# Optimization experiments

Hardware: AMD Instinct MI355X
Metric: run time of the kernel (lower is better)

Reference implementation:

```python
import jax, jax.numpy as jnp
import numpy as np

WINDOW = 32          # window_size
NUM_EIG = 8          # num_eigenvalues
EPS_NORM = 1e-8
EPS_DIV = 1e-8


def setup_inputs() -> dict:
    key = jax.random.key(0)
    h = jax.random.normal(key, (32, 4096, 1024), dtype=jnp.float32)
    return {"h": h}


def reference(h):
    batch, seq_len, hidden_dim = h.shape
    start = max(0, seq_len // 2 - 16)
    # [B, W, D] local window (fully in-bounds since seq_len >= window)
    w = jax.lax.dynamic_slice_in_dim(h, start, WINDOW, axis=1)
    wc = w - w.mean(axis=1, keepdims=True)                      # center over window
    wn = wc / (jnp.linalg.norm(wc, axis=2, keepdims=True) + EPS_NORM)
    # [B, W, W] local covariance (row-normalized gram)
    C = jnp.einsum('bwd,bvd->bwv', wn, wn)
    # batched symmetric eigendecomposition, ascending -> descending
    eigs = jnp.linalg.eigvalsh(C)[:, ::-1]                      # [B, W]
    e = eigs[:, :NUM_EIG + 1]                                    # top 9
    spectral_gap = e[:, NUM_EIG - 1] - e[:, NUM_EIG]             # lam_8 - lam_9
    decay_rate = (e[:, 0] - e[:, NUM_EIG]) / (NUM_EIG + 1)
    trace = jnp.trace(C, axis1=1, axis2=2)
    lambda_min = e[:, NUM_EIG] + 1e-8
    topo_term = jnp.maximum(spectral_gap / (decay_rate + EPS_DIV), 0.0)
    geo_term = lambda_min / (trace + EPS_DIV)
    gcve_scores = topo_term + geo_term                           # [B]
    fracture_scores = jnp.zeros_like(gcve_scores)                # phi_fn is None
    total_pressure = gcve_scores + fracture_scores
    return gcve_scores, fracture_scores, total_pressure
```

## Files before the change

kernel.cpp:

```cpp
#include <hip/hip_runtime.h>
#include <math.h>


namespace {
constexpr int HID = 1024;
constexpr int SEQ = 4096;
constexpr int START = 2032;
constexpr int NSWEEP = 8;

__device__ __forceinline__ void pairpq(int r, int m, int& p, int& q) {
    if (m == 0) { p = 31; q = r % 31; }
    else        { p = (r + m) % 31; q = (r + 31 - m) % 31; }
}
}

__global__ __launch_bounds__(256, 1)
void gyroid_probe_kernel(const float* __restrict__ h, float* __restrict__ out) {
    const int b = blockIdx.x;
    const int t = threadIdx.x;
    const float4* __restrict__ base4 =
        (const float4*)(h + ((size_t)b * SEQ + (size_t)START) * (size_t)HID);

    __shared__ float C[32][33];
    __shared__ __align__(16) float wcbuf[32][264];
    __shared__ float nsq[32];
    __shared__ float inv[32];
    __shared__ float csb[32];
    __shared__ float diag[32];
    __shared__ float misc[4];

    for (int i = t; i < 32 * 33; i += 256) (&C[0][0])[i] = 0.0f;
    if (t < 32) nsq[t] = 0.0f;
    if (t < 4)  misc[t] = 0.0f;
    __syncthreads();

    float4 sum4 = make_float4(0.f, 0.f, 0.f, 0.f);
    #pragma unroll
    for (int w = 0; w < 32; ++w) {
        float4 x = base4[w * 256 + t];
        sum4.x += x.x; sum4.y += x.y; sum4.z += x.z; sum4.w += x.w;
    }
    const float4 mean4 = make_float4(sum4.x * 0.03125f, sum4.y * 0.03125f,
                                     sum4.z * 0.03125f, sum4.w * 0.03125f);

    #pragma unroll
    for (int wi = 0; wi < 32; ++wi) {
        const int w = (wi + (t & 31)) & 31;
        float4 x = base4[w * 256 + t];
        const float dx = x.x - mean4.x, dy = x.y - mean4.y;
        const float dz = x.z - mean4.z, dw = x.w - mean4.w;
        atomicAdd(&nsq[w], dx * dx + dy * dy + dz * dz + dw * dw);
    }
    __syncthreads();

    const int tile = t & 15, kw = t >> 4;
    const int ti = tile >> 2, tj = tile & 3;
    float acc[8][8];
    #pragma unroll
    for (int i = 0; i < 8; ++i)
        #pragma unroll
        for (int j = 0; j < 8; ++j) acc[i][j] = 0.f;

    for (int g = 0; g < 4; ++g) {
        if ((t >> 6) == g) {
            const int col = t & 63;
            #pragma unroll
            for (int w = 0; w < 32; ++w) {
                float4 x = base4[w * 256 + t];
                float4 wc = make_float4(x.x - mean4.x, x.y - mean4.y,
                                        x.z - mean4.z, x.w - mean4.w);
                *(float4*)&wcbuf[w][col * 4] = wc;
            }
        }
        __syncthreads();
        #pragma unroll
        for (int k4 = 0; k4 < 4; ++k4) {
            const int k = kw * 16 + k4 * 4;
            float4 av[8], bv[8];
            #pragma unroll
            for (int i = 0; i < 8; ++i) av[i] = *(const float4*)&wcbuf[ti + 4 * i][k];
            #pragma unroll
            for (int j = 0; j < 8; ++j) bv[j] = *(const float4*)&wcbuf[tj + 4 * j][k];
            #pragma unroll
            for (int i = 0; i < 8; ++i)
                #pragma unroll
                for (int j = 0; j < 8; ++j)
                    acc[i][j] += av[i].x * bv[j].x + av[i].y * bv[j].y
                               + av[i].z * bv[j].z + av[i].w * bv[j].w;
        }
        __syncthreads();
    }

    #pragma unroll
    for (int i = 0; i < 8; ++i)
        #pragma unroll
        for (int j = 0; j < 8; ++j)
            atomicAdd(&C[ti + 4 * i][tj + 4 * j], acc[i][j]);
    __syncthreads();

    if (t < 32) inv[t] = 1.0f / (sqrtf(nsq[t]) + 1e-8f);
    __syncthreads();
    for (int i = t; i < 1024; i += 256) {
        const int w = i >> 5, v = i & 31;
        C[w][v] *= inv[w] * inv[v];
    }
    __syncthreads();
    if (t < 32) atomicAdd(&misc[0], C[t][t]);
    __syncthreads();

    for (int sweep = 0; sweep < NSWEEP; ++sweep) {
        for (int r = 0; r < 31; ++r) {
            if (t < 16) {
                int p, q; pairpq(r, t, p, q);
                const float app = C[p][p], aqq = C[q][q], apq = C[p][q];
                float cc = 1.f, ss = 0.f;
                if (fabsf(apq) > 1e-12f) {
                    const float tau = (aqq - app) / (2.f * apq);
                    float tt = 1.f / (fabsf(tau) + sqrtf(1.f + tau * tau));
                    if (tau < 0.f) tt = -tt;
                    cc = rsqrtf(1.f + tt * tt);
                    ss = tt * cc;
                }
                csb[t] = cc; csb[16 + t] = ss;
            }
            __syncthreads();
            {
                const int u = t >> 4, v = t & 15;
                int pu, qu, pv, qv;
                pairpq(r, u, pu, qu);
                pairpq(r, v, pv, qv);
                const float cu = csb[u], su = csb[16 + u];
                const float cv = csb[v], sv = csb[16 + v];
                const float a = C[pu][pv], bb = C[pu][qv];
                const float d = C[qu][pv], e = C[qu][qv];
                const float a1 = a * cv - bb * sv, b1 = a * sv + bb * cv;
                const float d1 = d * cv - e * sv,  e1 = d * sv + e * cv;
                C[pu][pv] = cu * a1 - su * d1;
                C[qu][pv] = su * a1 + cu * d1;
                C[pu][qv] = cu * b1 - su * e1;
                C[qu][qv] = su * b1 + cu * e1;
            }
            __syncthreads();
        }
    }

    if (t < 32) diag[t] = C[t][t];
    __syncthreads();
    if (t < 32) {
        const float dj = diag[t];
        int rank = 0;
        #pragma unroll
        for (int i = 0; i < 32; ++i) {
            const float di = diag[i];
            rank += (di > dj || (di == dj && i < t)) ? 1 : 0;
        }
        if (rank == 0) misc[1] = dj;
        if (rank == 7) misc[2] = dj;
        if (rank == 8) misc[3] = dj;
    }
    __syncthreads();

    if (t == 0) {
        const float tr = misc[0];
        const float e0 = misc[1], e7 = misc[2], e8 = misc[3];
        const float gap   = e7 - e8;
        const float decay = (e0 - e8) * (1.0f / 9.0f);
        const float lmin  = e8 + 1e-8f;
        const float topo  = fmaxf(gap / (decay + 1e-8f), 0.0f);
        const float geo   = lmin / (tr + 1e-8f);
        const float g     = topo + geo;
        out[b]      = g;
        out[32 + b] = 0.0f;
        out[64 + b] = g;
    }
}

extern "C" void kernel_launch(void* const* d_in, const int* in_sizes, int n_in,
                              void* d_out, int out_size, void* d_ws, size_t ws_size,
                              hipStream_t stream) {
    const float* h = (const float*)d_in[0];
    float* out = (float*)d_out;
    gyroid_probe_kernel<<<dim3(32), dim3(256), 0, stream>>>(h, out);
}
```

Measured before the change: 745.7 us.

## Cache window in registers, derive norms from Gram diagonal, single-wave Jacobi

The kernel now loads the 32-row window into registers once and centers it there, instead of reading global memory three times. Row norms come from the Gram matrix diagonal rather than a separate LDS-atomic pass. The Jacobi eigen-solve runs on a single 64-thread wavefront, so wave-level fences replace block-wide barriers, and the sweep count drops from 8 to 5. Holding 32 float4s per thread raises register pressure, and fewer sweeps may lose eigenvalue accuracy.

```diff
diff --git a/kernel.cpp b/kernel.cpp
--- a/kernel.cpp
+++ b/kernel.cpp
@@ -3,14 +3,18 @@
 
 
 namespace {
-constexpr int HID = 1024;
 constexpr int SEQ = 4096;
 constexpr int START = 2032;
-constexpr int NSWEEP = 8;
+constexpr int NSWEEP = 5;
 
 __device__ __forceinline__ void pairpq(int r, int m, int& p, int& q) {
     if (m == 0) { p = 31; q = r % 31; }
     else        { p = (r + m) % 31; q = (r + 31 - m) % 31; }
+}
+
+__device__ __forceinline__ void wavefence() {
+    __asm__ volatile("s_waitcnt lgkmcnt(0)" ::: "memory");
+    __builtin_amdgcn_wave_barrier();
 }
 }
 
@@ -19,37 +23,31 @@
     const int b = blockIdx.x;
     const int t = threadIdx.x;
     const float4* __restrict__ base4 =
-        (const float4*)(h + ((size_t)b * SEQ + (size_t)START) * (size_t)HID);
+        (const float4*)(h + ((size_t)b * SEQ + (size_t)START) * (size_t)1024);
 
     __shared__ float C[32][33];
     __shared__ __align__(16) float wcbuf[32][264];
-    __shared__ float nsq[32];
     __shared__ float inv[32];
     __shared__ float csb[32];
     __shared__ float diag[32];
     __shared__ float misc[4];
 
     for (int i = t; i < 32 * 33; i += 256) (&C[0][0])[i] = 0.0f;
-    if (t < 32) nsq[t] = 0.0f;
-    if (t < 4)  misc[t] = 0.0f;
-    __syncthreads();
+    if (t < 4) misc[t] = 0.0f;
 
-    float4 sum4 = make_float4(0.f, 0.f, 0.f, 0.f);
+    float4 xr[32];
+    #pragma unroll
+    for (int w = 0; w < 32; ++w) xr[w] = base4[w * 256 + t];
+    float4 s4 = make_float4(0.f, 0.f, 0.f, 0.f);
     #pragma unroll
     for (int w = 0; w < 32; ++w) {
-        float4 x = base4[w * 256 + t];
-        sum4.x += x.x; sum4.y += x.y; sum4.z += x.z; sum4.w += x.w;
+        s4.x += xr[w].x; s4.y += xr[w].y; s4.z += xr[w].z; s4.w += xr[w].w;
     }
-    const float4 mean4 = make_float4(sum4.x * 0.03125f, sum4.y * 0.03125f,
-                                     sum4.z * 0.03125f, sum4.w * 0.03125f);
-
+    const float4 m4 = make_float4(s4.x * 0.03125f, s4.y * 0.03125f,
+                                  s4.z * 0.03125f, s4.w * 0.03125f);
     #pragma unroll
-    for (int wi = 0; wi < 32; ++wi) {
-        const int w = (wi + (t & 31)) & 31;
-        float4 x = base4[w * 256 + t];
-        const float dx = x.x - mean4.x, dy = x.y - mean4.y;
-        const float dz = x.z - mean4.z, dw = x.w - mean4.w;
-        atomicAdd(&nsq[w], dx * dx + dy * dy + dz * dz + dw * dw);
+    for (int w = 0; w < 32; ++w) {
+        xr[w].x -= m4.x; xr[w].y -= m4.y; xr[w].z -= m4.z; xr[w].w -= m4.w;
     }
     __syncthreads();
 
@@ -65,12 +63,8 @@
         if ((t >> 6) == g) {
             const int col = t & 63;
             #pragma unroll
-            for (int w = 0; w < 32; ++w) {
-                float4 x = base4[w * 256 + t];
-                float4 wc = make_float4(x.x - mean4.x, x.y - mean4.y,
-                                        x.z - mean4.z, x.w - mean4.w);
-                *(float4*)&wcbuf[w][col * 4] = wc;
-            }
+            for (int w = 0; w < 32; ++w)
+                *(float4*)&wcbuf[w][col * 4] = xr[w];
         }
         __syncthreads();
         #pragma unroll
@@ -98,7 +92,7 @@
             atomicAdd(&C[ti + 4 * i][tj + 4 * j], acc[i][j]);
     __syncthreads();
 
-    if (t < 32) inv[t] = 1.0f / (sqrtf(nsq[t]) + 1e-8f);
+    if (t < 32) inv[t] = 1.0f / (sqrtf(C[t][t]) + 1e-8f);
     __syncthreads();
     for (int i = t; i < 1024; i += 256) {
         const int w = i >> 5, v = i & 31;
@@ -108,70 +102,74 @@
     if (t < 32) atomicAdd(&misc[0], C[t][t]);
     __syncthreads();
 
-    for (int sweep = 0; sweep < NSWEEP; ++sweep) {
-        for (int r = 0; r < 31; ++r) {
-            if (t < 16) {
-                int p, q; pairpq(r, t, p, q);
-                const float app = C[p][p], aqq = C[q][q], apq = C[p][q];
-                float cc = 1.f, ss = 0.f;
-                if (fabsf(apq) > 1e-12f) {
-                    const float tau = (aqq - app) / (2.f * apq);
-                    float tt = 1.f / (fabsf(tau) + sqrtf(1.f + tau * tau));
-                    if (tau < 0.f) tt = -tt;
-                    cc = rsqrtf(1.f + tt * tt);
-                    ss = tt * cc;
+    if (t < 64) {
+        const int v = t & 15, u0 = t >> 4;
+        for (int sweep = 0; sweep < NSWEEP; ++sweep) {
+            for (int r = 0; r < 31; ++r) {
+                if (t < 16) {
+                    int p, q; pairpq(r, t, p, q);
+                    const float app = C[p][p], aqq = C[q][q], apq = C[p][q];
+                    float cc = 1.f, ss = 0.f;
+                    if (fabsf(apq) > 1e-12f) {
+                        const float tau = (aqq - app) / (2.f * apq);
+                        float tt = 1.f / (fabsf(tau) + sqrtf(1.f + tau * tau));
+                        if (tau < 0.f) tt = -tt;
+                        cc = rsqrtf(1.f + tt * tt);
+                        ss = tt * cc;
+                    }
+                    csb[t] = cc; csb[16 + t] = ss;
                 }
-                csb[t] = cc; csb[16 + t] = ss;
+                wavefence();
+                {
+                    int pv, qv; pairpq(r, v, pv, qv);
+                    const float cv = csb[v], sv = csb[16 + v];
+                    #pragma unroll
+                    for (int kk = 0; kk < 4; ++kk) {
+                        const int u = u0 + 4 * kk;
+                        int pu, qu; pairpq(r, u, pu, qu);
+                        const float cu = csb[u], su = csb[16 + u];
+                        const float a = C[pu][pv], bb = C[pu][qv];
+                        const float d = C[qu][pv], e = C[qu][qv];
+                        const float a1 = a * cv - bb * sv, b1 = a * sv + bb * cv;
+                        const float d1 = d * cv - e * sv,  e1 = d * sv + e * cv;
+                        C[pu][pv] = cu * a1 - su * d1;
+                        C[qu][pv] = su * a1 + cu * d1;
+                        C[pu][qv] = cu * b1 - su * e1;
+                        C[qu][qv] = su * b1 + cu * e1;
+                    }
+                }
+                wavefence();
             }
-            __syncthreads();
-            {
-                const int u = t >> 4, v = t & 15;
-                int pu, qu, pv, qv;
-                pairpq(r, u, pu, qu);
-                pairpq(r, v, pv, qv);
-                const float cu = csb[u], su = csb[16 + u];
-                const float cv = csb[v], sv = csb[16 + v];
-                const float a = C[pu][pv], bb = C[pu][qv];
-                const float d = C[qu][pv], e = C[qu][qv];
-                const float a1 = a * cv - bb * sv, b1 = a * sv + bb * cv;
-                const float d1 = d * cv - e * sv,  e1 = d * sv + e * cv;
-                C[pu][pv] = cu * a1 - su * d1;
-                C[qu][pv] = su * a1 + cu * d1;
-                C[pu][qv] = cu * b1 - su * e1;
-                C[qu][qv] = su * b1 + cu * e1;
+        }
+
+        if (t < 32) diag[t] = C[t][t];
+        wavefence();
+        if (t < 32) {
+            const float dj = diag[t];
+            int rank = 0;
+            #pragma unroll
+            for (int i = 0; i < 32; ++i) {
+                const float di = diag[i];
+                rank += (di > dj || (di == dj && i < t)) ? 1 : 0;
             }
-            __syncthreads();
+            if (rank == 0) misc[1] = dj;
+            if (rank == 7) misc[2] = dj;
+            if (rank == 8) misc[3] = dj;
         }
-    }
-
-    if (t < 32) diag[t] = C[t][t];
-    __syncthreads();
-    if (t < 32) {
-        const float dj = diag[t];
-        int rank = 0;
-        #pragma unroll
-        for (int i = 0; i < 32; ++i) {
-            const float di = diag[i];
-            rank += (di > dj || (di == dj && i < t)) ? 1 : 0;
+        wavefence();
+        if (t == 0) {
+            const float tr = misc[0];
+            const float e0 = misc[1], e7 = misc[2], e8 = misc[3];
+            const float gap   = e7 - e8;
+            const float decay = (e0 - e8) * (1.0f / 9.0f);
+            const float lmin  = e8 + 1e-8f;
+            const float topo  = fmaxf(gap / (decay + 1e-8f), 0.0f);
+            const float geo   = lmin / (tr + 1e-8f);
+            const float g     = topo + geo;
+            out[b]      = g;
+            out[32 + b] = 0.0f;
+            out[64 + b] = g;
         }
-        if (rank == 0) misc[1] = dj;
-        if (rank == 7) misc[2] = dj;
-        if (rank == 8) misc[3] = dj;
-    }
-    __syncthreads();
-
-    if (t == 0) {
-        const float tr = misc[0];
-        const float e0 = misc[1], e7 = misc[2], e8 = misc[3];
-        const float gap   = e7 - e8;
-        const float decay = (e0 - e8) * (1.0f / 9.0f);
-        const float lmin  = e8 + 1e-8f;
-        const float topo  = fmaxf(gap / (decay + 1e-8f), 0.0f);
-        const float geo   = lmin / (tr + 1e-8f);
-        const float g     = topo + geo;
-        out[b]      = g;
-        out[32 + b] = 0.0f;
-        out[64 + b] = g;
     }
 }
 
```

New measurement: 722.2 us. 3.2% less time.
